# Kernel tuning notes

Hardware: AMD Instinct MI355X
Metric: run time of the kernel (lower is better)

The kernel has to match this reference:

```python
import jax, jax.numpy as jnp
import numpy as np
from jax import lax

WARMUP = 365
X1S = (100.0, 1200.0); X2S = (-5.0, 3.0); X3S = (20.0, 300.0); X4S = (1.1, 2.9)
K1, K2 = 3, 6  # max UH kernel lengths: ceil(x4_max)=3, ceil(2*x4_max)=6


def _uh_kernels(x4):
    # x4: [B]. S-curve differences, padded with zeros beyond ceil(x4)/ceil(2*x4).
    t1 = jnp.arange(K1 + 1, dtype=x4.dtype)
    sh1 = jnp.minimum(t1[None, :] / x4[:, None], 1.0) ** 2.5          # [B, K1+1]
    uh1 = sh1[:, 1:] - sh1[:, :-1]                                     # [B, K1]
    t2 = jnp.arange(K2 + 1, dtype=x4.dtype)
    r = t2[None, :] / x4[:, None]
    sh2 = jnp.where(t2[None, :] <= x4[:, None],
                    0.5 * r ** 2.5,
                    1.0 - 0.5 * jnp.maximum(2.0 - r, 0.0) ** 2.5)      # [B, K2+1]
    uh2 = sh2[:, 1:] - sh2[:, :-1]                                     # [B, K2]
    return uh1, uh2


def _causal_conv(x, uh):
    # x: [T, B], uh: [B, K] -> y[t,b] = sum_k uh[b,k] * x[t-k,b]
    T = x.shape[0]
    out = jnp.zeros_like(x)
    for k in range(uh.shape[1]):  # K is small and static (<=6)
        shifted = jnp.pad(x, ((k, 0), (0, 0)))[:T]
        out = out + uh[:, k][None, :] * shifted
    return out


def _gr4j_core(p_and_e, x1, x2, x3, x4, s0, r0):
    # p_and_e: [T, B, 2]
    diff = p_and_e[:, :, 0] - p_and_e[:, :, 1]
    pn = jnp.maximum(diff, 0.0)   # net precip [T, B]
    en = jnp.maximum(-diff, 0.0)  # net evap   [T, B]

    def prod_step(s, pe):
        p, e = pe
        s = jnp.clip(s, 0.0, x1)
        tp = jnp.tanh(p / x1)
        te = jnp.tanh(e / x1)
        ps = x1 * (1.0 - (s / x1) ** 2) * tp / (1.0 + s / x1 * tp)
        es = s * (2.0 - s / x1) * te / (1.0 + (1.0 - s / x1) * te)
        s2 = jnp.clip(s - es + ps, 0.0, x1)
        perc = s2 * (1.0 - (1.0 + (4.0 / 9.0 * s2 / x1) ** 4) ** (-0.25))
        s2 = s2 - perc
        pr = perc + (pn_step := p - ps) * 1.0 + 0.0 * pn_step  # pr = perc + (pn - ps)
        return s2, pr

    s_final, prs = lax.scan(prod_step, s0, (pn, en))  # prs: [T, B]

    uh1, uh2 = _uh_kernels(x4)
    q9 = _causal_conv(prs, uh1)  # [T, B]
    q1 = _causal_conv(prs, uh2)  # [T, B]

    def route_step(r, q):
        q9t, q1t = q
        r = jnp.clip(r, 0.0, x3)
        gex = x2 * (r / x3) ** 3.5
        r2 = jnp.maximum(0.0, r + q9t + gex)
        qr = r2 * (1.0 - (1.0 + (r2 / x3) ** 4) ** (-0.25))
        r2 = r2 - qr
        qd = jnp.maximum(0.0, q1t + gex)
        return r2, qr + qd

    r_final, q = lax.scan(route_step, r0, (q9, q1))  # q: [T, B]
    return q, s_final, r_final


def _forward(p_and_e, parameters):
    x1 = X1S[0] + parameters[:, 0] * (X1S[1] - X1S[0])
    x2 = X2S[0] + parameters[:, 1] * (X2S[1] - X2S[0])
    x3 = X3S[0] + parameters[:, 2] * (X3S[1] - X3S[0])
    x4 = X4S[0] + parameters[:, 3] * (X4S[1] - X4S[0])
    if WARMUP > 0:
        # warmup runs under no_grad in torch: stop gradients through it
        _, s_w, r_w = _gr4j_core(p_and_e[:WARMUP], x1, x2, x3, x4,
                                 0.5 * lax.stop_gradient(x1),
                                 0.5 * lax.stop_gradient(x3))
        s0 = lax.stop_gradient(s_w)
        r0 = lax.stop_gradient(r_w)
    else:
        s0 = 0.5 * lax.stop_gradient(x1)
        r0 = 0.5 * lax.stop_gradient(x3)
    q, _, _ = _gr4j_core(p_and_e[WARMUP:], x1, x2, x3, x4, s0, r0)
    return q[:, :, None]  # [T-WARMUP, B, 1]


def setup_inputs() -> dict:
    key = jax.random.key(0)
    k1, k2 = jax.random.split(key)
    p_and_e = jax.random.uniform(k1, (4015, 2048, 2), dtype=jnp.float32)
    parameters = jax.random.uniform(k2, (2048, 4), dtype=jnp.float32)
    return {"p_and_e": p_and_e, "parameters": parameters}


def reference(p_and_e, parameters):
    return _forward(p_and_e, parameters)
```

## Files before the change

kernel.cpp:

```cpp
#include <hip/hip_runtime.h>


#define T_TOTAL 4015
#define NWARM   365
#define NB      2048
#define BSTEP   55
#define NBATCH  73

__global__ __launch_bounds__(128, 1)
void gr4j_kernel(const float2* __restrict__ pe_in,
                 const float*  __restrict__ params,
                 float*        __restrict__ out)
{
    const int lane = threadIdx.x & 63;
    const int wid  = threadIdx.x >> 6;
    const int b    = blockIdx.x * 64 + lane;

    __shared__ float prbuf[2][BSTEP * 64];

    const float x1 = 100.0f + params[b * 4 + 0] * 1100.0f;
    const float x2 = -5.0f  + params[b * 4 + 1] * 8.0f;
    const float x3 = 20.0f  + params[b * 4 + 2] * 280.0f;
    const float x4 = 1.1f   + params[b * 4 + 3] * 1.8f;
    const float invx1 = __builtin_amdgcn_rcpf(x1);
    const float invx3 = __builtin_amdgcn_rcpf(x3);
    const float c49   = (4.0f / 9.0f) * invx1;
    const float c49_2 = c49 * c49;
    const float c4s   = c49_2 * c49_2;
    const float i3_2  = invx3 * invx3;
    const float c4r   = i3_2 * i3_2;

    float u10, u11, u12, u20, u21, u22, u23, u24, u25;
    {
        float sh[3];
        #pragma unroll
        for (int j = 1; j <= 3; ++j)
            sh[j - 1] = powf(fminf((float)j / x4, 1.0f), 2.5f);
        u10 = sh[0]; u11 = sh[1] - sh[0]; u12 = sh[2] - sh[1];
        float s2h[6];
        #pragma unroll
        for (int j = 1; j <= 6; ++j) {
            float rr = (float)j / x4;
            s2h[j - 1] = ((float)j <= x4) ? 0.5f * powf(rr, 2.5f)
                       : 1.0f - 0.5f * powf(fmaxf(2.0f - rr, 0.0f), 2.5f);
        }
        u20 = s2h[0];          u21 = s2h[1] - s2h[0]; u22 = s2h[2] - s2h[1];
        u23 = s2h[3] - s2h[2]; u24 = s2h[4] - s2h[3]; u25 = s2h[5] - s2h[4];
    }

    float s = 0.5f * x1;
    float r = 0.5f * x3;
    float ph0 = 0.f, ph1 = 0.f, ph2 = 0.f, ph3 = 0.f, ph4 = 0.f;

    auto prod_step = [&](float2 pe) -> float {
        const float diff = pe.x - pe.y;
        const float pn = fmaxf(diff, 0.0f);
        const float en = fmaxf(-diff, 0.0f);
        const float ap = pn * invx1;
        const float ae = en * invx1;
        const float sx = s * invx1;
        const float dp = fmaf(sx, ap, 1.0f);
        const float de = fmaf(1.0f - sx, ae, 1.0f);
        const float n1 = fmaf(-sx, sx, 1.0f);
        const float nump = pn * n1;
        const float nume = (sx * en) * (2.0f - sx);
        const float rpe = __builtin_amdgcn_rcpf(dp * de);
        const float a_ = nump * de;
        const float b_ = nume * dp;
        const float s2 = fmaf(a_ - b_, rpe, s);
        const float ps = a_ * rpe;
        const float s22 = s2 * s2;
        const float s24 = s22 * s22;
        const float z = c4s * s24;
        float w = fmaf(z, 15.0f / 128.0f, -5.0f / 32.0f);
        w = fmaf(z, w, 0.25f);
        const float perc = (s2 * z) * w;
        s = s2 - perc;
        return perc + (pn - ps);
    };

    auto w1_step = [&](float pr) -> float {
        const float q9 = fmaf(u10, pr, fmaf(u11, ph0, u12 * ph1));
        const float q1 = fmaf(u20, pr, fmaf(u21, ph0, fmaf(u22, ph1,
                         fmaf(u23, ph2, fmaf(u24, ph3, u25 * ph4)))));
        ph4 = ph3; ph3 = ph2; ph2 = ph1; ph1 = ph0; ph0 = pr;
        const float rx = r * invx3;
        const float srx = __builtin_amdgcn_sqrtf(rx);
        const float gex = (x2 * ((rx * rx) * rx)) * srx;
        const float r2 = fmaxf(0.0f, (r + q9) + gex);
        const float r22 = r2 * r2;
        const float r24 = r22 * r22;
        const float v4p1 = fmaf(c4r, r24, 1.0f);
        const float rn = r2 * __builtin_amdgcn_rsqf(__builtin_amdgcn_sqrtf(v4p1));
        const float qr = r2 - rn;
        r = rn;
        return qr + fmaxf(0.0f, q1 + gex);
    };

    const float2* gptr = pe_in + b;
    float2 rot[11];
    if (wid == 0) {
        #pragma unroll
        for (int i = 0; i < 11; ++i) rot[i] = gptr[(size_t)i * NB];
    }

    for (int k = 0; k <= NBATCH; ++k) {
        if (wid == 0) {
            if (k < NBATCH) {
                const int tb = k * BSTEP;
                float* dst = &prbuf[k & 1][0] + lane;
                const int grf = (k < NBATCH - 1) ? 5 : 4;
                for (int g = 0; g < 5; ++g) {
                    float* d2 = dst + g * (11 * 64);
                    if (g < grf) {
                        const float2* gp = gptr + (size_t)(tb + g * 11 + 11) * NB;
                        #pragma unroll
                        for (int i = 0; i < 11; ++i) {
                            const float2 pe = rot[i];
                            rot[i] = gp[(size_t)i * NB];
                            d2[i * 64] = prod_step(pe);
                        }
                    } else {
                        #pragma unroll
                        for (int i = 0; i < 11; ++i)
                            d2[i * 64] = prod_step(rot[i]);
                    }
                }
            }
        } else if (k >= 1) {
            const int kb = k - 1;
            const float* src = &prbuf[kb & 1][0] + lane;
            if (kb != 6) {
                float* ob = (kb < 6)
                    ? out + (size_t)(kb * BSTEP) * NB + b
                    : out + (size_t)(kb * BSTEP - NWARM) * NB + b;
                float prr[11];
                #pragma unroll
                for (int i = 0; i < 11; ++i) prr[i] = src[i * 64];
                for (int g = 0; g < 5; ++g) {
                    const float* sp = src + (g + 1) * (11 * 64);
                    float* ob2 = ob + (size_t)(g * 11) * NB;
                    if (g < 4) {
                        #pragma unroll
                        for (int i = 0; i < 11; ++i) {
                            const float pr = prr[i];
                            prr[i] = sp[i * 64];
                            ob2[(size_t)i * NB] = w1_step(pr);
                        }
                    } else {
                        #pragma unroll
                        for (int i = 0; i < 11; ++i)
                            ob2[(size_t)i * NB] = w1_step(prr[i]);
                    }
                }
            } else {
                float* dumpb = out + (size_t)330 * NB + b;
                float* realb = out + b;
                float prr[11];
                #pragma unroll
                for (int i = 0; i < 11; ++i) prr[i] = src[i * 64];
                #pragma unroll
                for (int g = 0; g < 5; ++g) {
                    #pragma unroll
                    for (int i = 0; i < 11; ++i) {
                        const int j = g * 11 + i;
                        const float pr = prr[i];
                        if (g < 4) prr[i] = src[(j + 11) * 64];
                        if (j == 35) { ph0 = ph1 = ph2 = ph3 = ph4 = 0.0f; }
                        const float q = w1_step(pr);
                        if (j < 35) dumpb[(size_t)j * NB] = q;
                        else        realb[(size_t)(j - 35) * NB] = q;
                    }
                }
            }
        }
        __syncthreads();
    }
}

extern "C" void kernel_launch(void* const* d_in, const int* in_sizes, int n_in,
                              void* d_out, int out_size, void* d_ws, size_t ws_size,
                              hipStream_t stream) {
    const float2* pe_in  = (const float2*)d_in[0];
    const float*  params = (const float*)d_in[1];
    float* out = (float*)d_out;
    (void)in_sizes; (void)n_in; (void)out_size; (void)d_ws; (void)ws_size;

    gr4j_kernel<<<dim3(NB / 64), dim3(128), 0, stream>>>(pe_in, params, out);
}
```

Measured before the change: 404.3 us.

## Replace per-batch barriers with LDS flag handshake between producer and consumer waves

The production wave and the routing wave now coordinate through shared-memory produced/consumed counters with acquire/release atomics and spin-waits, instead of a block-wide __syncthreads after every batch. This removes lockstep barriers so each wave can run ahead by up to one double-buffer slot, absorbing timing differences between the two stages. It also splits the per-wave state so each wave only holds its own variables, which may lower register pressure. The risk is the cost of spin-polling LDS and the correctness of the memory ordering for LDS data across waves.

```diff
diff --git a/kernel.cpp b/kernel.cpp
--- a/kernel.cpp
+++ b/kernel.cpp
@@ -17,6 +17,10 @@
     const int b    = blockIdx.x * 64 + lane;
 
     __shared__ float prbuf[2][BSTEP * 64];
+    __shared__ int produced;
+    __shared__ int consumed;
+    if (threadIdx.x == 0) { produced = 0; consumed = 0; }
+    __syncthreads();
 
     const float x1 = 100.0f + params[b * 4 + 0] * 1100.0f;
     const float x2 = -5.0f  + params[b * 4 + 1] * 8.0f;
@@ -30,110 +34,117 @@
     const float i3_2  = invx3 * invx3;
     const float c4r   = i3_2 * i3_2;
 
-    float u10, u11, u12, u20, u21, u22, u23, u24, u25;
-    {
-        float sh[3];
-        #pragma unroll
-        for (int j = 1; j <= 3; ++j)
-            sh[j - 1] = powf(fminf((float)j / x4, 1.0f), 2.5f);
-        u10 = sh[0]; u11 = sh[1] - sh[0]; u12 = sh[2] - sh[1];
-        float s2h[6];
-        #pragma unroll
-        for (int j = 1; j <= 6; ++j) {
-            float rr = (float)j / x4;
-            s2h[j - 1] = ((float)j <= x4) ? 0.5f * powf(rr, 2.5f)
-                       : 1.0f - 0.5f * powf(fmaxf(2.0f - rr, 0.0f), 2.5f);
-        }
-        u20 = s2h[0];          u21 = s2h[1] - s2h[0]; u22 = s2h[2] - s2h[1];
-        u23 = s2h[3] - s2h[2]; u24 = s2h[4] - s2h[3]; u25 = s2h[5] - s2h[4];
-    }
-
-    float s = 0.5f * x1;
-    float r = 0.5f * x3;
-    float ph0 = 0.f, ph1 = 0.f, ph2 = 0.f, ph3 = 0.f, ph4 = 0.f;
-
-    auto prod_step = [&](float2 pe) -> float {
-        const float diff = pe.x - pe.y;
-        const float pn = fmaxf(diff, 0.0f);
-        const float en = fmaxf(-diff, 0.0f);
-        const float ap = pn * invx1;
-        const float ae = en * invx1;
-        const float sx = s * invx1;
-        const float dp = fmaf(sx, ap, 1.0f);
-        const float de = fmaf(1.0f - sx, ae, 1.0f);
-        const float n1 = fmaf(-sx, sx, 1.0f);
-        const float nump = pn * n1;
-        const float nume = (sx * en) * (2.0f - sx);
-        const float rpe = __builtin_amdgcn_rcpf(dp * de);
-        const float a_ = nump * de;
-        const float b_ = nume * dp;
-        const float s2 = fmaf(a_ - b_, rpe, s);
-        const float ps = a_ * rpe;
-        const float s22 = s2 * s2;
-        const float s24 = s22 * s22;
-        const float z = c4s * s24;
-        float w = fmaf(z, 15.0f / 128.0f, -5.0f / 32.0f);
-        w = fmaf(z, w, 0.25f);
-        const float perc = (s2 * z) * w;
-        s = s2 - perc;
-        return perc + (pn - ps);
-    };
-
-    auto w1_step = [&](float pr) -> float {
-        const float q9 = fmaf(u10, pr, fmaf(u11, ph0, u12 * ph1));
-        const float q1 = fmaf(u20, pr, fmaf(u21, ph0, fmaf(u22, ph1,
-                         fmaf(u23, ph2, fmaf(u24, ph3, u25 * ph4)))));
-        ph4 = ph3; ph3 = ph2; ph2 = ph1; ph1 = ph0; ph0 = pr;
-        const float rx = r * invx3;
-        const float srx = __builtin_amdgcn_sqrtf(rx);
-        const float gex = (x2 * ((rx * rx) * rx)) * srx;
-        const float r2 = fmaxf(0.0f, (r + q9) + gex);
-        const float r22 = r2 * r2;
-        const float r24 = r22 * r22;
-        const float v4p1 = fmaf(c4r, r24, 1.0f);
-        const float rn = r2 * __builtin_amdgcn_rsqf(__builtin_amdgcn_sqrtf(v4p1));
-        const float qr = r2 - rn;
-        r = rn;
-        return qr + fmaxf(0.0f, q1 + gex);
-    };
-
-    const float2* gptr = pe_in + b;
-    float2 rot[11];
     if (wid == 0) {
+        float s = 0.5f * x1;
+
+        auto prod_step = [&](float2 pe) -> float {
+            const float diff = pe.x - pe.y;
+            const float pn = fmaxf(diff, 0.0f);
+            const float en = fmaxf(-diff, 0.0f);
+            const float ap = pn * invx1;
+            const float ae = en * invx1;
+            const float sx = s * invx1;
+            const float dp = fmaf(sx, ap, 1.0f);
+            const float de = fmaf(1.0f - sx, ae, 1.0f);
+            const float n1 = fmaf(-sx, sx, 1.0f);
+            const float nump = pn * n1;
+            const float nume = (sx * en) * (2.0f - sx);
+            const float rpe = __builtin_amdgcn_rcpf(dp * de);
+            const float a_ = nump * de;
+            const float b_ = nume * dp;
+            const float s2 = fmaf(a_ - b_, rpe, s);
+            const float ps = a_ * rpe;
+            const float s22 = s2 * s2;
+            const float s24 = s22 * s22;
+            const float z = c4s * s24;
+            float w = fmaf(z, 15.0f / 128.0f, -5.0f / 32.0f);
+            w = fmaf(z, w, 0.25f);
+            const float perc = (s2 * z) * w;
+            s = s2 - perc;
+            return perc + (pn - ps);
+        };
+
+        const float2* gptr = pe_in + b;
+        float2 rot[11];
         #pragma unroll
         for (int i = 0; i < 11; ++i) rot[i] = gptr[(size_t)i * NB];
-    }
-
-    for (int k = 0; k <= NBATCH; ++k) {
-        if (wid == 0) {
-            if (k < NBATCH) {
-                const int tb = k * BSTEP;
-                float* dst = &prbuf[k & 1][0] + lane;
-                const int grf = (k < NBATCH - 1) ? 5 : 4;
-                for (int g = 0; g < 5; ++g) {
-                    float* d2 = dst + g * (11 * 64);
-                    if (g < grf) {
-                        const float2* gp = gptr + (size_t)(tb + g * 11 + 11) * NB;
-                        #pragma unroll
-                        for (int i = 0; i < 11; ++i) {
-                            const float2 pe = rot[i];
-                            rot[i] = gp[(size_t)i * NB];
-                            d2[i * 64] = prod_step(pe);
-                        }
-                    } else {
-                        #pragma unroll
-                        for (int i = 0; i < 11; ++i)
-                            d2[i * 64] = prod_step(rot[i]);
+
+        for (int k = 0; k < NBATCH; ++k) {
+            if (k >= 2) {
+                while (__hip_atomic_load(&consumed, __ATOMIC_ACQUIRE,
+                                         __HIP_MEMORY_SCOPE_WORKGROUP) < k - 1) {}
+            }
+            float* dst = &prbuf[k & 1][0] + lane;
+            const int tb = k * BSTEP;
+            const int grf = (k < NBATCH - 1) ? 5 : 4;
+            for (int g = 0; g < 5; ++g) {
+                float* d2 = dst + g * (11 * 64);
+                if (g < grf) {
+                    const float2* gp = gptr + (size_t)(tb + g * 11 + 11) * NB;
+                    #pragma unroll
+                    for (int i = 0; i < 11; ++i) {
+                        const float2 pe = rot[i];
+                        rot[i] = gp[(size_t)i * NB];
+                        d2[i * 64] = prod_step(pe);
                     }
+                } else {
+                    #pragma unroll
+                    for (int i = 0; i < 11; ++i)
+                        d2[i * 64] = prod_step(rot[i]);
                 }
             }
-        } else if (k >= 1) {
-            const int kb = k - 1;
-            const float* src = &prbuf[kb & 1][0] + lane;
-            if (kb != 6) {
-                float* ob = (kb < 6)
-                    ? out + (size_t)(kb * BSTEP) * NB + b
-                    : out + (size_t)(kb * BSTEP - NWARM) * NB + b;
+            __hip_atomic_store(&produced, k + 1, __ATOMIC_RELEASE,
+                               __HIP_MEMORY_SCOPE_WORKGROUP);
+        }
+    } else {
+        float u10, u11, u12, u20, u21, u22, u23, u24, u25;
+        {
+            float sh[3];
+            #pragma unroll
+            for (int j = 1; j <= 3; ++j)
+                sh[j - 1] = powf(fminf((float)j / x4, 1.0f), 2.5f);
+            u10 = sh[0]; u11 = sh[1] - sh[0]; u12 = sh[2] - sh[1];
+            float s2h[6];
+            #pragma unroll
+            for (int j = 1; j <= 6; ++j) {
+                float rr = (float)j / x4;
+                s2h[j - 1] = ((float)j <= x4) ? 0.5f * powf(rr, 2.5f)
+                           : 1.0f - 0.5f * powf(fmaxf(2.0f - rr, 0.0f), 2.5f);
+            }
+            u20 = s2h[0];          u21 = s2h[1] - s2h[0]; u22 = s2h[2] - s2h[1];
+            u23 = s2h[3] - s2h[2]; u24 = s2h[4] - s2h[3]; u25 = s2h[5] - s2h[4];
+        }
+
+        float r = 0.5f * x3;
+        float ph0 = 0.f, ph1 = 0.f, ph2 = 0.f, ph3 = 0.f, ph4 = 0.f;
+
+        auto w1_step = [&](float pr) -> float {
+            const float q9 = fmaf(u10, pr, fmaf(u11, ph0, u12 * ph1));
+            const float q1 = fmaf(u20, pr, fmaf(u21, ph0, fmaf(u22, ph1,
+                             fmaf(u23, ph2, fmaf(u24, ph3, u25 * ph4)))));
+            ph4 = ph3; ph3 = ph2; ph2 = ph1; ph1 = ph0; ph0 = pr;
+            const float rq = r + q9;
+            const float rx = r * invx3;
+            const float srx = __builtin_amdgcn_sqrtf(rx);
+            const float gex = (x2 * ((rx * rx) * rx)) * srx;
+            const float r2 = fmaxf(0.0f, rq + gex);
+            const float r22 = r2 * r2;
+            const float r24 = r22 * r22;
+            const float v4p1 = fmaf(c4r, r24, 1.0f);
+            const float rn = r2 * __builtin_amdgcn_rsqf(__builtin_amdgcn_sqrtf(v4p1));
+            const float qr = r2 - rn;
+            r = rn;
+            return qr + fmaxf(0.0f, q1 + gex);
+        };
+
+        for (int k = 0; k < NBATCH; ++k) {
+            while (__hip_atomic_load(&produced, __ATOMIC_ACQUIRE,
+                                     __HIP_MEMORY_SCOPE_WORKGROUP) < k + 1) {}
+            const float* src = &prbuf[k & 1][0] + lane;
+            if (k != 6) {
+                float* ob = (k < 6)
+                    ? out + (size_t)(k * BSTEP) * NB + b
+                    : out + (size_t)(k * BSTEP - NWARM) * NB + b;
                 float prr[11];
                 #pragma unroll
                 for (int i = 0; i < 11; ++i) prr[i] = src[i * 64];
@@ -173,8 +184,9 @@
                     }
                 }
             }
+            __hip_atomic_store(&consumed, k + 1, __ATOMIC_RELEASE,
+                               __HIP_MEMORY_SCOPE_WORKGROUP);
         }
-        __syncthreads();
     }
 }
 
```

After: 400.3 us. Within noise of the previous version (-1.0%).
